# Kernel tuning notes

Measured on AMD Instinct MI355X. Metric: run time of the kernel, lower is better.

## Reference

```python
import jax, jax.numpy as jnp
import numpy as np

B, T, I, H, O = 8, 4096, 128, 256, 64
H2 = 2 * H  # bidirectional feature size


def _init(key, shape, scale):
    return (jax.random.uniform(key, shape, jnp.float32) * 2.0 - 1.0) * scale


def setup_inputs() -> dict:
    key = jax.random.key(0)
    ks = jax.random.split(key, 14)
    s = 1.0 / np.sqrt(H)  # torch GRU init scale
    return {
        "x": jax.random.normal(ks[0], (B, T, I), jnp.float32),
        # forward-direction GRU params (gate order: r, z, n)
        "w_ih_f": _init(ks[1], (3 * H, I), s),
        "w_hh_f": _init(ks[2], (3 * H, H), s),
        "b_ih_f": _init(ks[3], (3 * H,), s),
        "b_hh_f": _init(ks[4], (3 * H,), s),
        # backward-direction GRU params
        "w_ih_b": _init(ks[5], (3 * H, I), s),
        "w_hh_b": _init(ks[6], (3 * H, H), s),
        "b_ih_b": _init(ks[7], (3 * H,), s),
        "b_hh_b": _init(ks[8], (3 * H,), s),
        # attention params
        "w_att": jax.random.normal(ks[9], (H2, H2), jnp.float32) * (1.0 / np.sqrt(H2)),
        "v_att": jax.random.normal(ks[10], (H2, 1), jnp.float32) * (1.0 / np.sqrt(H2)),
        # output linear
        "w_lin": _init(ks[11], (O, H2), 1.0 / np.sqrt(H2)),
        "b_lin": _init(ks[12], (O,), 1.0 / np.sqrt(H2)),
    }


def _run_gru(x, w_ih, w_hh, b_ih, b_hh, reverse):
    # x: [B,T,I] -> outputs [B,T,H]. PyTorch GRU cell math, gates ordered r,z,n.
    gx = jnp.einsum("bti,gi->btg", x, w_ih) + b_ih  # precompute input gates [B,T,3H]
    gx = jnp.moveaxis(gx, 1, 0)  # [T,B,3H] for scan

    def step(h, gxt):
        gh = h @ w_hh.T + b_hh  # [B,3H]
        xr, xz, xn = jnp.split(gxt, 3, axis=-1)
        hr, hz, hn = jnp.split(gh, 3, axis=-1)
        r = jax.nn.sigmoid(xr + hr)
        z = jax.nn.sigmoid(xz + hz)
        n = jnp.tanh(xn + r * hn)
        h_new = (1.0 - z) * n + z * h
        return h_new, h_new

    h0 = jnp.zeros((x.shape[0], w_hh.shape[1]), x.dtype)
    _, hs = jax.lax.scan(step, h0, gx, reverse=reverse)  # outputs time-aligned
    return jnp.moveaxis(hs, 0, 1)  # [B,T,H]


def reference(x, w_ih_f, w_hh_f, b_ih_f, b_hh_f, w_ih_b, w_hh_b, b_ih_b, b_hh_b,
              w_att, v_att, w_lin, b_lin):
    hf = _run_gru(x, w_ih_f, w_hh_f, b_ih_f, b_hh_f, reverse=False)
    hb = _run_gru(x, w_ih_b, w_hh_b, b_ih_b, b_hh_b, reverse=True)
    pred = jnp.concatenate([hf, hb], axis=-1)  # [B,T,2H]
    # attention over time: fused replacement of per-timestep mm/cat loops
    squish = jnp.tanh(jnp.einsum("bth,hk->btk", pred, w_att))  # [B,T,2H]
    scores = jnp.einsum("btk,k->bt", squish, v_att[:, 0])  # [B,T]
    a = jax.nn.softmax(scores, axis=-1)  # [B,T]
    ctx = jnp.einsum("bt,bth->bh", a, pred)  # [B,2H]
    logits = ctx @ w_lin.T + b_lin  # [B,O]
    return jax.nn.softmax(logits, axis=-1)
```

## Files before the change

kernel.cpp:

```cpp
#include <hip/hip_runtime.h>
#include <cstdint>
#include <cstddef>

#define NB 8
#define NT 4096
#define NI 128
#define NH 256
#define NH2 512
#define NO 64
#define NSLICE 8
#define NJS 32

#define OFF_H64   0
#define OFF_SC    16384
#define OFF_CTX   49152
#define OFF_WT    53248
#define OFF_PRED  315392
#define ZERO_FLOATS 53248

__global__ __launch_bounds__(384, 1) void gru_rec(
    const float* __restrict__ x,
    const float* __restrict__ w_ih_f, const float* __restrict__ w_hh_f,
    const float* __restrict__ b_ih_f, const float* __restrict__ b_hh_f,
    const float* __restrict__ w_ih_b, const float* __restrict__ w_hh_b,
    const float* __restrict__ b_ih_b, const float* __restrict__ b_hh_b,
    unsigned long long* __restrict__ hbuf, float* __restrict__ pred)
{
    const int wg = blockIdx.x;
    const int dir = wg & 1;
    const int bb = (wg >> 1) & 7;
    const int slice = wg >> 4;
    const int tid = threadIdx.x;
    const int row = tid >> 2;
    const int q = tid & 3;
    const int g = row >> 5;
    const int jj = row & 31;
    const int grow = g * NH + slice * NJS + jj;

    const float* wih = dir ? w_ih_b : w_ih_f;
    const float* whh = dir ? w_hh_b : w_hh_f;
    const float* bih = dir ? b_ih_b : b_ih_f;
    const float* bhh = dir ? b_hh_b : b_hh_f;

    float wh[64], wi[32];
    {
        const float* p = whh + (size_t)grow * NH + q * 64;
        #pragma unroll
        for (int i = 0; i < 16; ++i) {
            float4 v = *(const float4*)(p + i * 4);
            wh[4*i] = v.x; wh[4*i+1] = v.y; wh[4*i+2] = v.z; wh[4*i+3] = v.w;
        }
        const float* p2 = wih + (size_t)grow * NI + q * 32;
        #pragma unroll
        for (int i = 0; i < 8; ++i) {
            float4 v = *(const float4*)(p2 + i * 4);
            wi[4*i] = v.x; wi[4*i+1] = v.y; wi[4*i+2] = v.z; wi[4*i+3] = v.w;
        }
    }
    const float bi = bih[grow];
    const float bh = bhh[grow];

    __shared__ float h_lds[268];
    __shared__ float x_lds[140];
    __shared__ float gx_l[96], gh_l[96];

    unsigned long long* hb = hbuf + (size_t)(dir * NB + bb) * 2 * NH;
    const float* xb = x + (size_t)bb * NT * NI;
    float* predb = pred + (size_t)bb * NT * NH2 + dir * NH;

    const int xc = tid - NH;
    float xreg = 0.f;
    if (tid >= NH) {
        const int t0 = dir ? (NT - 1) : 0;
        xreg = xb[(size_t)t0 * NI + xc];
    }

    for (int s = 0; s < NT; ++s) {
        const int t = dir ? (NT - 1 - s) : s;
        const int pr = s & 1, pw = pr ^ 1;

        if (tid < NH) {
            const unsigned long long* ap = hb + pr * NH + tid;
            unsigned long long pk;
            do {
                pk = __hip_atomic_load(ap, __ATOMIC_RELAXED, __HIP_MEMORY_SCOPE_AGENT);
            } while ((unsigned)(pk >> 32) != (unsigned)s);
            h_lds[tid + 4 * (tid >> 6)] = __uint_as_float((unsigned)pk);
        } else {
            x_lds[xc + 4 * (xc >> 5)] = xreg;
        }
        __syncthreads();

        float ah = 0.f, ax = 0.f;
        {
            const float* hp = h_lds + q * 68;
            #pragma unroll
            for (int i = 0; i < 64; ++i) ah += wh[i] * hp[i];
            const float* xp = x_lds + q * 36;
            #pragma unroll
            for (int i = 0; i < 32; ++i) ax += wi[i] * xp[i];
        }
        ah += __shfl_xor(ah, 1); ah += __shfl_xor(ah, 2);
        ax += __shfl_xor(ax, 1); ax += __shfl_xor(ax, 2);
        if (q == 0) { gx_l[row] = ax + bi; gh_l[row] = ah + bh; }
        if (tid >= NH && s + 1 < NT) {
            const int tn = dir ? (NT - 2 - s) : (s + 1);
            xreg = xb[(size_t)tn * NI + xc];
        }
        __syncthreads();

        if (tid < NJS) {
            const float xr = gx_l[tid],      hr = gh_l[tid];
            const float xz = gx_l[32 + tid], hz = gh_l[32 + tid];
            const float xn = gx_l[64 + tid], hn = gh_l[64 + tid];
            const float r = 1.f / (1.f + __expf(-(xr + hr)));
            const float z = 1.f / (1.f + __expf(-(xz + hz)));
            const float n = tanhf(xn + r * hn);
            const int c = slice * NJS + tid;
            const float hold = h_lds[c + 4 * (c >> 6)];
            const float hnew = (1.f - z) * n + z * hold;
            predb[(size_t)t * NH2 + c] = hnew;
            const unsigned long long pk =
                ((unsigned long long)(unsigned)(s + 1) << 32) |
                (unsigned long long)__float_as_uint(hnew);
            __hip_atomic_store(hb + pw * NH + c, pk,
                               __ATOMIC_RELAXED, __HIP_MEMORY_SCOPE_AGENT);
        }
        __syncthreads();
    }
}

__global__ void transpose_watt(const float* __restrict__ w_att, float* __restrict__ wT) {
    const int n = blockIdx.x * 256 + threadIdx.x;
    const int k = n >> 9, h = n & 511;
    wT[n] = w_att[h * NH2 + k];
}

__global__ __launch_bounds__(256) void scores_gemm(
    const float* __restrict__ pred, const float* __restrict__ wT,
    const float* __restrict__ v_att, float* __restrict__ scores)
{
    const int tt = blockIdx.x, kt = blockIdx.y, bb = blockIdx.z;
    const int tid = threadIdx.x;
    const int tx = tid & 15;
    const int ty = tid >> 4;
    __shared__ float As[64][68];
    __shared__ float Bs[64][68];
    __shared__ float red[64][17];
    float acc[4][4] = {{0.f}};
    const int t0 = tt * 64, k0 = kt * 64;
    const float* pb = pred + ((size_t)bb * NT + t0) * NH2;

    for (int hc = 0; hc < NH2; hc += 64) {
        #pragma unroll
        for (int r = 0; r < 4; ++r) {
            const int idx = tid + 256 * r;
            const int tr = idx >> 4;
            const int c4 = (idx & 15) * 4;
            float4 a = *(const float4*)(pb + (size_t)tr * NH2 + hc + c4);
            *(float4*)&As[tr][c4] = a;
            float4 w = *(const float4*)(wT + (size_t)(k0 + tr) * NH2 + hc + c4);
            Bs[c4 + 0][tr] = w.x; Bs[c4 + 1][tr] = w.y;
            Bs[c4 + 2][tr] = w.z; Bs[c4 + 3][tr] = w.w;
        }
        __syncthreads();
        #pragma unroll
        for (int h = 0; h < 64; ++h) {
            const float a0 = As[ty*4+0][h], a1 = As[ty*4+1][h];
            const float a2 = As[ty*4+2][h], a3 = As[ty*4+3][h];
            const float4 bv = *(const float4*)&Bs[h][tx*4];
            acc[0][0] += a0*bv.x; acc[0][1] += a0*bv.y; acc[0][2] += a0*bv.z; acc[0][3] += a0*bv.w;
            acc[1][0] += a1*bv.x; acc[1][1] += a1*bv.y; acc[1][2] += a1*bv.z; acc[1][3] += a1*bv.w;
            acc[2][0] += a2*bv.x; acc[2][1] += a2*bv.y; acc[2][2] += a2*bv.z; acc[2][3] += a2*bv.w;
            acc[3][0] += a3*bv.x; acc[3][1] += a3*bv.y; acc[3][2] += a3*bv.z; acc[3][3] += a3*bv.w;
        }
        __syncthreads();
    }
    const float4 vv = *(const float4*)(v_att + k0 + tx * 4);
    #pragma unroll
    for (int i = 0; i < 4; ++i) {
        const float p = tanhf(acc[i][0]) * vv.x + tanhf(acc[i][1]) * vv.y
                      + tanhf(acc[i][2]) * vv.z + tanhf(acc[i][3]) * vv.w;
        red[ty*4+i][tx] = p;
    }
    __syncthreads();
    if (tid < 64) {
        float ssum = 0.f;
        #pragma unroll
        for (int xx = 0; xx < 16; ++xx) ssum += red[tid][xx];
        atomicAdd(&scores[bb * NT + t0 + tid], ssum);
    }
}

__global__ void softmax_t(float* __restrict__ scores) {
    const int bb = blockIdx.x;
    const int tid = threadIdx.x;
    __shared__ float red[256];
    float m = -1e30f;
    for (int t = tid; t < NT; t += 256) m = fmaxf(m, scores[bb*NT + t]);
    red[tid] = m; __syncthreads();
    for (int s2 = 128; s2; s2 >>= 1) { if (tid < s2) red[tid] = fmaxf(red[tid], red[tid+s2]); __syncthreads(); }
    m = red[0]; __syncthreads();
    float sum = 0.f;
    for (int t = tid; t < NT; t += 256) sum += expf(scores[bb*NT + t] - m);
    red[tid] = sum; __syncthreads();
    for (int s2 = 128; s2; s2 >>= 1) { if (tid < s2) red[tid] += red[tid+s2]; __syncthreads(); }
    const float inv = 1.f / red[0];
    for (int t = tid; t < NT; t += 256) scores[bb*NT + t] = expf(scores[bb*NT + t] - m) * inv;
}

__global__ void ctx_kernel(const float* __restrict__ pred, const float* __restrict__ a,
                           float* __restrict__ ctx) {
    const int bb = blockIdx.x, ch = blockIdx.y;
    const int tid = threadIdx.x;
    const int t0 = ch * 128;
    float acc0 = 0.f, acc1 = 0.f;
    for (int t = 0; t < 128; ++t) {
        const float av = a[bb*NT + t0 + t];
        const float* p = pred + ((size_t)bb * NT + t0 + t) * NH2;
        acc0 += av * p[tid];
        acc1 += av * p[tid + 256];
    }
    atomicAdd(&ctx[bb*NH2 + tid], acc0);
    atomicAdd(&ctx[bb*NH2 + tid + 256], acc1);
}

__global__ __launch_bounds__(512) void final_kernel(
    const float* __restrict__ ctx, const float* __restrict__ w_lin,
    const float* __restrict__ b_lin, float* __restrict__ out)
{
    const int tid = threadIdx.x;
    const int bb = tid >> 6, o = tid & 63;
    __shared__ float cl[NB][NH2];
    for (int i = tid; i < NB * NH2; i += 512) cl[i >> 9][i & 511] = ctx[i];
    __syncthreads();
    float acc = b_lin[o];
    for (int h = 0; h < NH2; h += 4) {
        const float4 w = *(const float4*)&w_lin[o * NH2 + h];
        acc += cl[bb][h]*w.x + cl[bb][h+1]*w.y + cl[bb][h+2]*w.z + cl[bb][h+3]*w.w;
    }
    float m = acc;
    for (int off = 32; off; off >>= 1) m = fmaxf(m, __shfl_xor(m, off));
    const float e = expf(acc - m);
    float ssum = e;
    for (int off = 32; off; off >>= 1) ssum += __shfl_xor(ssum, off);
    out[tid] = e / ssum;
}

extern "C" void kernel_launch(void* const* d_in, const int* in_sizes, int n_in,
                              void* d_out, int out_size, void* d_ws, size_t ws_size,
                              hipStream_t stream) {
    (void)in_sizes; (void)n_in; (void)out_size; (void)ws_size;
    const float* x      = (const float*)d_in[0];
    const float* w_ih_f = (const float*)d_in[1];
    const float* w_hh_f = (const float*)d_in[2];
    const float* b_ih_f = (const float*)d_in[3];
    const float* b_hh_f = (const float*)d_in[4];
    const float* w_ih_b = (const float*)d_in[5];
    const float* w_hh_b = (const float*)d_in[6];
    const float* b_ih_b = (const float*)d_in[7];
    const float* b_hh_b = (const float*)d_in[8];
    const float* w_att  = (const float*)d_in[9];
    const float* v_att  = (const float*)d_in[10];
    const float* w_lin  = (const float*)d_in[11];
    const float* b_lin  = (const float*)d_in[12];

    float* ws     = (float*)d_ws;
    unsigned long long* hbuf = (unsigned long long*)(ws + OFF_H64);
    float* scores = ws + OFF_SC;
    float* ctx    = ws + OFF_CTX;
    float* wT     = ws + OFF_WT;
    float* pred   = ws + OFF_PRED;
    float* out    = (float*)d_out;

    hipMemsetAsync(d_ws, 0, (size_t)ZERO_FLOATS * sizeof(float), stream);
    hipLaunchKernelGGL(transpose_watt, dim3(1024), dim3(256), 0, stream, w_att, wT);
    hipLaunchKernelGGL(gru_rec, dim3(128), dim3(384), 0, stream,
                       x, w_ih_f, w_hh_f, b_ih_f, b_hh_f,
                       w_ih_b, w_hh_b, b_ih_b, b_hh_b, hbuf, pred);
    hipLaunchKernelGGL(scores_gemm, dim3(64, 8, 8), dim3(256), 0, stream,
                       pred, wT, v_att, scores);
    hipLaunchKernelGGL(softmax_t, dim3(8), dim3(256), 0, stream, scores);
    hipLaunchKernelGGL(ctx_kernel, dim3(8, 32), dim3(256), 0, stream, pred, scores, ctx);
    hipLaunchKernelGGL(final_kernel, dim3(1), dim3(512), 0, stream, ctx, w_lin, b_lin, out);
}
```

Measured before the change: 5.666 ms.

## Restructure GRU recurrence: two barriers per step, local h reuse, cache-hinted polling

Reorders the per-step loop so gate finalization, the cross-workgroup hidden-state exchange and the x prefetch happen in one phase, followed by the matvec phase. This cuts barriers per step from three to two. Each slice now keeps its own new h in a register and LDS instead of rereading it from global memory, and only polls the other 224 entries. Publication uses inline-asm stores with sc0/sc1 cache bits and polling uses sc0 loads, falling back to agent-scope atomics after ten tries. It also swaps tanhf for an exp-based formula. The hand-written cache-coherence asm risks subtle memory-ordering bugs.

```diff
diff --git a/kernel.cpp b/kernel.cpp
--- a/kernel.cpp
+++ b/kernel.cpp
@@ -17,6 +17,19 @@
 #define OFF_WT    53248
 #define OFF_PRED  315392
 #define ZERO_FLOATS 53248
+
+__device__ __forceinline__ void st_l2(unsigned long long* p, unsigned long long v) {
+    asm volatile("global_store_dwordx2 %0, %1, off sc0" :: "v"(p), "v"(v) : "memory");
+}
+__device__ __forceinline__ void st_if(unsigned long long* p, unsigned long long v) {
+    asm volatile("global_store_dwordx2 %0, %1, off sc0 sc1" :: "v"(p), "v"(v) : "memory");
+}
+__device__ __forceinline__ unsigned long long ld_l2(const unsigned long long* p) {
+    unsigned long long v;
+    asm volatile("global_load_dwordx2 %0, %1, off sc0\n\ts_waitcnt vmcnt(0)"
+                 : "=v"(v) : "v"(p) : "memory");
+    return v;
+}
 
 __global__ __launch_bounds__(384, 1) void gru_rec(
     const float* __restrict__ x,
@@ -68,65 +81,102 @@
     const float* xb = x + (size_t)bb * NT * NI;
     float* predb = pred + (size_t)bb * NT * NH2 + dir * NH;
 
-    const int xc = tid - NH;
-    float xreg = 0.f;
-    if (tid >= NH) {
-        const int t0 = dir ? (NT - 1) : 0;
-        xreg = xb[(size_t)t0 * NI + xc];
-    }
-
-    for (int s = 0; s < NT; ++s) {
-        const int t = dir ? (NT - 1 - s) : s;
-        const int pr = s & 1, pw = pr ^ 1;
-
-        if (tid < NH) {
-            const unsigned long long* ap = hb + pr * NH + tid;
+    if (tid < NH) h_lds[tid + 4 * (tid >> 6)] = 0.f;
+    float hprev = 0.f;
+    float xr0 = 0.f, xr1 = 0.f;
+    if (tid >= 320) {
+        const int i0 = tid - 320;
+        const int t1 = dir ? (NT - 1) : 0;
+        xr0 = xb[(size_t)t1 * NI + i0];
+        xr1 = xb[(size_t)t1 * NI + i0 + 64];
+        x_lds[i0 + 4 * (i0 >> 5)] = xr0;
+        { const int c1 = i0 + 64; x_lds[c1 + 4 * (c1 >> 5)] = xr1; }
+        const int t2 = dir ? (NT - 2) : 1;
+        xr0 = xb[(size_t)t2 * NI + i0];
+        xr1 = xb[(size_t)t2 * NI + i0 + 64];
+    }
+    __syncthreads();
+
+    {
+        float ah = 0.f, ax = 0.f;
+        const float* hp = h_lds + q * 68;
+        #pragma unroll
+        for (int i = 0; i < 64; ++i) ah += wh[i] * hp[i];
+        const float* xp = x_lds + q * 36;
+        #pragma unroll
+        for (int i = 0; i < 32; ++i) ax += wi[i] * xp[i];
+        ah += __shfl_xor(ah, 1); ah += __shfl_xor(ah, 2);
+        ax += __shfl_xor(ax, 1); ax += __shfl_xor(ax, 2);
+        if (q == 0) { gx_l[row] = ax + bi; gh_l[row] = ah + bh; }
+    }
+    __syncthreads();
+
+    for (int k = 1; k <= NT; ++k) {
+        const int tcur = dir ? (NT - k) : (k - 1);
+
+        if (tid < NJS) {
+            const float xr = gx_l[tid],      hr = gh_l[tid];
+            const float xz = gx_l[32 + tid], hz = gh_l[32 + tid];
+            const float xn = gx_l[64 + tid], hn = gh_l[64 + tid];
+            const float r = 1.f / (1.f + __expf(-(xr + hr)));
+            const float z = 1.f / (1.f + __expf(-(xz + hz)));
+            const float y = xn + r * hn;
+            const float e2 = __expf(-2.f * y);
+            const float n = (1.f - e2) / (1.f + e2);
+            const float hnew = (1.f - z) * n + z * hprev;
+            const int c = slice * NJS + tid;
+            predb[(size_t)tcur * NH2 + c] = hnew;
+            const unsigned long long pk =
+                ((unsigned long long)(unsigned)k << 32) |
+                (unsigned long long)__float_as_uint(hnew);
+            unsigned long long* slot = hb + (size_t)(k & 1) * NH + c;
+            st_l2(slot, pk);
+            st_if(slot, pk);
+            h_lds[c + 4 * (c >> 6)] = hnew;
+            hprev = hnew;
+        } else if (tid >= 64 && tid < 288) {
+            const int idx = tid - 64;
+            const int rc = idx < slice * NJS ? idx : idx + NJS;
+            const unsigned long long* ap = hb + (size_t)(k & 1) * NH + rc;
+            const unsigned tag = (unsigned)k;
             unsigned long long pk;
-            do {
-                pk = __hip_atomic_load(ap, __ATOMIC_RELAXED, __HIP_MEMORY_SCOPE_AGENT);
-            } while ((unsigned)(pk >> 32) != (unsigned)s);
-            h_lds[tid + 4 * (tid >> 6)] = __uint_as_float((unsigned)pk);
-        } else {
-            x_lds[xc + 4 * (xc >> 5)] = xreg;
+            int tries = 0;
+            for (;;) {
+                pk = ld_l2(ap);
+                if ((unsigned)(pk >> 32) == tag) break;
+                if (++tries > 10) {
+                    do {
+                        pk = __hip_atomic_load(ap, __ATOMIC_RELAXED,
+                                               __HIP_MEMORY_SCOPE_AGENT);
+                    } while ((unsigned)(pk >> 32) != tag);
+                    break;
+                }
+            }
+            h_lds[rc + 4 * (rc >> 6)] = __uint_as_float((unsigned)pk);
+        } else if (tid >= 320) {
+            const int i0 = tid - 320;
+            x_lds[i0 + 4 * (i0 >> 5)] = xr0;
+            { const int c1 = i0 + 64; x_lds[c1 + 4 * (c1 >> 5)] = xr1; }
+            int tn = dir ? (NT - (k + 2)) : (k + 1);
+            tn = tn < 0 ? 0 : (tn >= NT ? NT - 1 : tn);
+            xr0 = xb[(size_t)tn * NI + i0];
+            xr1 = xb[(size_t)tn * NI + i0 + 64];
         }
         __syncthreads();
 
-        float ah = 0.f, ax = 0.f;
-        {
+        if (k < NT) {
+            float ah = 0.f, ax = 0.f;
             const float* hp = h_lds + q * 68;
             #pragma unroll
             for (int i = 0; i < 64; ++i) ah += wh[i] * hp[i];
             const float* xp = x_lds + q * 36;
             #pragma unroll
             for (int i = 0; i < 32; ++i) ax += wi[i] * xp[i];
-        }
-        ah += __shfl_xor(ah, 1); ah += __shfl_xor(ah, 2);
-        ax += __shfl_xor(ax, 1); ax += __shfl_xor(ax, 2);
-        if (q == 0) { gx_l[row] = ax + bi; gh_l[row] = ah + bh; }
-        if (tid >= NH && s + 1 < NT) {
-            const int tn = dir ? (NT - 2 - s) : (s + 1);
-            xreg = xb[(size_t)tn * NI + xc];
-        }
-        __syncthreads();
-
-        if (tid < NJS) {
-            const float xr = gx_l[tid],      hr = gh_l[tid];
-            const float xz = gx_l[32 + tid], hz = gh_l[32 + tid];
-            const float xn = gx_l[64 + tid], hn = gh_l[64 + tid];
-            const float r = 1.f / (1.f + __expf(-(xr + hr)));
-            const float z = 1.f / (1.f + __expf(-(xz + hz)));
-            const float n = tanhf(xn + r * hn);
-            const int c = slice * NJS + tid;
-            const float hold = h_lds[c + 4 * (c >> 6)];
-            const float hnew = (1.f - z) * n + z * hold;
-            predb[(size_t)t * NH2 + c] = hnew;
-            const unsigned long long pk =
-                ((unsigned long long)(unsigned)(s + 1) << 32) |
-                (unsigned long long)__float_as_uint(hnew);
-            __hip_atomic_store(hb + pw * NH + c, pk,
-                               __ATOMIC_RELAXED, __HIP_MEMORY_SCOPE_AGENT);
-        }
-        __syncthreads();
+            ah += __shfl_xor(ah, 1); ah += __shfl_xor(ah, 2);
+            ax += __shfl_xor(ax, 1); ax += __shfl_xor(ax, 2);
+            if (q == 0) { gx_l[row] = ax + bi; gh_l[row] = ah + bh; }
+            __syncthreads();
+        }
     }
 }
 
```

New measurement: 7.959 ms. +40.5%, slower.

## Add XCC-local fast path for cross-workgroup hidden-state exchange

Applied to the files above, without the earlier changes.

At startup, each group of workgroups that share one (direction, batch) recurrence reads the hardware XCC id and checks whether all of its slices sit on the same XCC. If they do, hidden-state polling uses a plain store and an sc0 global load that is served from the shared L2 instead of device-scope atomics. Every value is also written to a mirror buffer with agent-scope atomics, and a reader falls back to that buffer after a few failed tries. The aim is lower per-timestep synchronisation latency on the serial recurrence, at the cost of an extra store and a setup handshake. The change also replaces tanhf with an exp-based formula.

```diff
diff --git a/kernel.cpp b/kernel.cpp
--- a/kernel.cpp
+++ b/kernel.cpp
@@ -12,11 +12,23 @@
 #define NJS 32
 
 #define OFF_H64   0
-#define OFF_SC    16384
-#define OFF_CTX   49152
-#define OFF_WT    53248
-#define OFF_PRED  315392
-#define ZERO_FLOATS 53248
+#define OFF_MIR   16384
+#define OFF_XCC   32768
+#define OFF_SC    33024
+#define OFF_CTX   65792
+#define OFF_WT    69888
+#define OFF_PRED  332032
+#define ZERO_FLOATS 69888
+
+__device__ __forceinline__ void st_plain(unsigned long long* p, unsigned long long v) {
+    asm volatile("global_store_dwordx2 %0, %1, off" :: "v"(p), "v"(v) : "memory");
+}
+__device__ __forceinline__ unsigned long long ld_l2(const unsigned long long* p) {
+    unsigned long long v;
+    asm volatile("global_load_dwordx2 %0, %1, off sc0\n\ts_waitcnt vmcnt(0)"
+                 : "=v"(v) : "v"(p) : "memory");
+    return v;
+}
 
 __global__ __launch_bounds__(384, 1) void gru_rec(
     const float* __restrict__ x,
@@ -24,7 +36,8 @@
     const float* __restrict__ b_ih_f, const float* __restrict__ b_hh_f,
     const float* __restrict__ w_ih_b, const float* __restrict__ w_hh_b,
     const float* __restrict__ b_ih_b, const float* __restrict__ b_hh_b,
-    unsigned long long* __restrict__ hbuf, float* __restrict__ pred)
+    unsigned long long* __restrict__ hbuf, unsigned long long* __restrict__ mir,
+    unsigned long long* __restrict__ xccbuf, float* __restrict__ pred)
 {
     const int wg = blockIdx.x;
     const int dir = wg & 1;
@@ -63,8 +76,32 @@
     __shared__ float h_lds[268];
     __shared__ float x_lds[140];
     __shared__ float gx_l[96], gh_l[96];
+    __shared__ int fast_flag;
+
+    if (tid == 0) {
+        unsigned xcc;
+        asm volatile("s_getreg_b32 %0, hwreg(HW_REG_XCC_ID)" : "=s"(xcc));
+        xcc &= 0xFu;
+        unsigned long long* xb64 = xccbuf + (size_t)(wg & 15) * NSLICE;
+        __hip_atomic_store(&xb64[slice],
+                           (1ull << 32) | (unsigned long long)xcc,
+                           __ATOMIC_RELAXED, __HIP_MEMORY_SCOPE_AGENT);
+        int same = 1;
+        for (int p = 0; p < NSLICE; ++p) {
+            unsigned long long pk;
+            do {
+                pk = __hip_atomic_load(&xb64[p], __ATOMIC_RELAXED,
+                                       __HIP_MEMORY_SCOPE_AGENT);
+            } while ((unsigned)(pk >> 32) != 1u);
+            same &= ((unsigned)pk == xcc);
+        }
+        fast_flag = same;
+    }
+    __syncthreads();
+    bool use_fast = (fast_flag != 0);
 
     unsigned long long* hb = hbuf + (size_t)(dir * NB + bb) * 2 * NH;
+    unsigned long long* mb = mir  + (size_t)(dir * NB + bb) * 2 * NH;
     const float* xb = x + (size_t)bb * NT * NI;
     float* predb = pred + (size_t)bb * NT * NH2 + dir * NH;
 
@@ -80,11 +117,25 @@
         const int pr = s & 1, pw = pr ^ 1;
 
         if (tid < NH) {
-            const unsigned long long* ap = hb + pr * NH + tid;
-            unsigned long long pk;
-            do {
-                pk = __hip_atomic_load(ap, __ATOMIC_RELAXED, __HIP_MEMORY_SCOPE_AGENT);
-            } while ((unsigned)(pk >> 32) != (unsigned)s);
+            const unsigned tag = (unsigned)s;
+            unsigned long long pk = 0;
+            bool got = false;
+            if (use_fast) {
+                const unsigned long long* fp = hb + pr * NH + tid;
+                #pragma unroll 1
+                for (int tries = 0; tries < 8; ++tries) {
+                    pk = ld_l2(fp);
+                    if ((unsigned)(pk >> 32) == tag) { got = true; break; }
+                }
+                if (!got) use_fast = false;
+            }
+            if (!got) {
+                const unsigned long long* mp = mb + pr * NH + tid;
+                do {
+                    pk = __hip_atomic_load(mp, __ATOMIC_RELAXED,
+                                           __HIP_MEMORY_SCOPE_AGENT);
+                } while ((unsigned)(pk >> 32) != tag);
+            }
             h_lds[tid + 4 * (tid >> 6)] = __uint_as_float((unsigned)pk);
         } else {
             x_lds[xc + 4 * (xc >> 5)] = xreg;
@@ -115,7 +166,9 @@
             const float xn = gx_l[64 + tid], hn = gh_l[64 + tid];
             const float r = 1.f / (1.f + __expf(-(xr + hr)));
             const float z = 1.f / (1.f + __expf(-(xz + hz)));
-            const float n = tanhf(xn + r * hn);
+            const float y = xn + r * hn;
+            const float e2 = __expf(-2.f * y);
+            const float n = (1.f - e2) / (1.f + e2);
             const int c = slice * NJS + tid;
             const float hold = h_lds[c + 4 * (c >> 6)];
             const float hnew = (1.f - z) * n + z * hold;
@@ -123,7 +176,8 @@
             const unsigned long long pk =
                 ((unsigned long long)(unsigned)(s + 1) << 32) |
                 (unsigned long long)__float_as_uint(hnew);
-            __hip_atomic_store(hb + pw * NH + c, pk,
+            st_plain(hb + pw * NH + c, pk);
+            __hip_atomic_store(mb + pw * NH + c, pk,
                                __ATOMIC_RELAXED, __HIP_MEMORY_SCOPE_AGENT);
         }
         __syncthreads();
@@ -267,6 +321,8 @@
 
     float* ws     = (float*)d_ws;
     unsigned long long* hbuf = (unsigned long long*)(ws + OFF_H64);
+    unsigned long long* mir  = (unsigned long long*)(ws + OFF_MIR);
+    unsigned long long* xcc  = (unsigned long long*)(ws + OFF_XCC);
     float* scores = ws + OFF_SC;
     float* ctx    = ws + OFF_CTX;
     float* wT     = ws + OFF_WT;
@@ -277,7 +333,7 @@
     hipLaunchKernelGGL(transpose_watt, dim3(1024), dim3(256), 0, stream, w_att, wT);
     hipLaunchKernelGGL(gru_rec, dim3(128), dim3(384), 0, stream,
                        x, w_ih_f, w_hh_f, b_ih_f, b_hh_f,
-                       w_ih_b, w_hh_b, b_ih_b, b_hh_b, hbuf, pred);
+                       w_ih_b, w_hh_b, b_ih_b, b_hh_b, hbuf, mir, xcc, pred);
     hipLaunchKernelGGL(scores_gemm, dim3(64, 8, 8), dim3(256), 0, stream,
                        pred, wT, v_att, scores);
     hipLaunchKernelGGL(softmax_t, dim3(8), dim3(256), 0, stream, scores);
```

New measurement: 6.135 ms. 8.3% more time.
